# Kernel tuning notes

Hardware: AMD Instinct MI355X
Metric: run time of the kernel (lower is better)

The kernel has to match this reference:

```python
import jax, jax.numpy as jnp
import numpy as np

B, C, Himg, Wimg = 32, 256, 64, 64
P = 8            # partition (window) size
HEADS, DH = 8, 32
SEQ = P * P      # tokens per window = 64
SCALE = C ** (-0.5)  # note: feat_dim**-0.5, as in the source
EPS = 1e-5


def _relative_position_index(h, w):
    coords = np.stack(np.meshgrid(np.arange(h), np.arange(w), indexing='ij'))  # [2,h,w]
    cf = coords.reshape(2, -1)
    rel = cf[:, :, None] - cf[:, None, :]            # [2,hw,hw]
    rel = rel.transpose(1, 2, 0)
    rel[:, :, 0] += h - 1
    rel[:, :, 1] += w - 1
    rel[:, :, 0] *= 2 * w - 1
    return rel.sum(-1)                               # [hw,hw] int

REL_IDX = jnp.asarray(_relative_position_index(P, P).reshape(-1))  # [SEQ*SEQ]


def layernorm(x, g, b):
    mu = jnp.mean(x, -1, keepdims=True)
    var = jnp.mean(jnp.square(x - mu), -1, keepdims=True)
    return (x - mu) * jax.lax.rsqrt(var + EPS) * g + b


def setup_inputs() -> dict:
    key = jax.random.key(0)
    ks = jax.random.split(key, 12)
    d = {}
    d['x'] = jax.random.normal(ks[0], (B, C, Himg, Wimg), jnp.float32)
    d['ln1_g'] = jnp.ones((C,), jnp.float32)
    d['ln1_b'] = jnp.zeros((C,), jnp.float32)
    d['qkv_w'] = jax.random.normal(ks[1], (C, 3 * C), jnp.float32) * 0.02
    d['qkv_b'] = jnp.zeros((3 * C,), jnp.float32)
    d['merge_w'] = jax.random.normal(ks[2], (C, C), jnp.float32) * 0.02
    d['merge_b'] = jnp.zeros((C,), jnp.float32)
    d['bias_table'] = jax.random.normal(ks[3], ((2 * P - 1) * (2 * P - 1), HEADS), jnp.float32) * 0.02
    d['ln2_g'] = jnp.ones((C,), jnp.float32)
    d['ln2_b'] = jnp.zeros((C,), jnp.float32)
    d['mlp_w1'] = jax.random.normal(ks[4], (C, 4 * C), jnp.float32) * 0.02
    d['mlp_b1'] = jnp.zeros((4 * C,), jnp.float32)
    d['mlp_w2'] = jax.random.normal(ks[5], (4 * C, C), jnp.float32) * 0.02
    d['mlp_b2'] = jnp.zeros((C,), jnp.float32)
    return d


def reference(x, ln1_g, ln1_b, qkv_w, qkv_b, merge_w, merge_b, bias_table,
              ln2_g, ln2_b, mlp_w1, mlp_b1, mlp_w2, mlp_b2):
    Bn, Cn, H, W = x.shape
    hp, wp = H // P, W // P
    # window partition: [B,C,H,W] -> [B, G, P*P, C]
    xw = x.reshape(Bn, Cn, hp, P, wp, P).transpose(0, 2, 4, 3, 5, 1)
    xw = xw.reshape(Bn, hp * wp, P * P, Cn)

    # --- attention block ---
    h = layernorm(xw, ln1_g, ln1_b)
    qkv = h @ qkv_w + qkv_b                                    # [B,G,S,3C]
    q, k, v = jnp.split(qkv, 3, axis=-1)
    def heads(t):
        return t.reshape(Bn, hp * wp, SEQ, HEADS, DH).transpose(0, 1, 3, 2, 4)
    q, k, v = heads(q), heads(k) * SCALE, heads(v)             # [B,G,h,S,d]
    scores = jnp.einsum('bghid,bghjd->bghij', q, k)            # [B,G,h,S,S]
    rel_bias = bias_table[REL_IDX].reshape(SEQ, SEQ, HEADS).transpose(2, 0, 1)
    attn = jax.nn.softmax(scores + rel_bias[None, None], axis=-1)
    out = jnp.einsum('bghij,bghjd->bghid', attn, v)            # [B,G,h,S,d]
    out = out.transpose(0, 1, 3, 2, 4).reshape(Bn, hp * wp, SEQ, Cn)
    xw = xw + (out @ merge_w + merge_b)

    # --- MLP block ---
    h = layernorm(xw, ln2_g, ln2_b)
    h = jax.nn.gelu(h @ mlp_w1 + mlp_b1, approximate=False)
    xw = xw + (h @ mlp_w2 + mlp_b2)

    # window departition: [B,G,P*P,C] -> [B,C,H,W]
    y = xw.reshape(Bn, hp, wp, P, P, Cn).transpose(0, 5, 1, 3, 2, 4)
    return y.reshape(Bn, Cn, hp * P, wp * P)
```

## Files before the change

kernel.cpp:

```cpp
#include <hip/hip_runtime.h>

typedef __attribute__((ext_vector_type(8))) short short8;
typedef __attribute__((ext_vector_type(4))) short short4v;
typedef __attribute__((ext_vector_type(8))) unsigned short ushort8v;
typedef __attribute__((ext_vector_type(4))) float f32x4;
typedef __attribute__((ext_vector_type(4))) int int4v;
typedef __attribute__((ext_vector_type(4))) unsigned short ushort4v;
typedef __attribute__((ext_vector_type(2))) unsigned short ushort2v;

#define SCALE_F 0.0625f
#define EPS_F 1e-5f

__device__ __forceinline__ float bf2f(unsigned short u) {
  unsigned int i = ((unsigned int)u) << 16;
  return __builtin_bit_cast(float, i);
}
__device__ __forceinline__ unsigned short f2bf(float f) {
  unsigned int i = __builtin_bit_cast(unsigned int, f);
  i += 0x7fffu + ((i >> 16) & 1u);
  return (unsigned short)(i >> 16);
}

__device__ __forceinline__ float fast_gelu(float v) {
  float s = v * v;
  float u = v * __builtin_fmaf(s, 0.0713548163f, 1.5957691216f);
  float e = __expf(u);
  float r = __builtin_amdgcn_rcpf(e + 1.f);
  return v - v * r;
}

__device__ __forceinline__ void gload_lds16(const unsigned short* g, unsigned short* l) {
  __builtin_amdgcn_global_load_lds(
      (const __attribute__((address_space(1))) void*)g,
      (__attribute__((address_space(3))) void*)l, 16, 0, 0);
}

template<int K, int N>
__global__ void cast_wt(const float* __restrict__ src, unsigned short* __restrict__ dst) {
  int id = blockIdx.x * 256 + threadIdx.x;
  if (id >= K * N) return;
  int k = id % K, n = id / K;
  dst[id] = f2bf(src[(size_t)k * N + n]);
}

__global__ void build_relb(const float* __restrict__ table, float* __restrict__ relb) {
  int id = blockIdx.x * 256 + threadIdx.x;
  int h = id >> 12, i = (id >> 6) & 63, j = id & 63;
  int dy = (i >> 3) - (j >> 3) + 7;
  int dx = (i & 7) - (j & 7) + 7;
  relb[id] = table[(dy * 15 + dx) * 8 + h];
}

#define PLN_RS 264
__global__ __launch_bounds__(256) void part_ln1(
    const float* __restrict__ x, const float* __restrict__ g, const float* __restrict__ bb,
    unsigned short* __restrict__ h) {
  __shared__ __align__(16) unsigned short t_lds[128 * PLN_RS];
  __shared__ float ps_sum[128][2];
  __shared__ float ps_ss[128][2];
  const int tid = threadIdx.x;
  const int bid = blockIdx.x;
  const int b = bid >> 5, wr = (bid >> 2) & 7, cp = bid & 3;
  const int r0 = wr * 8;
  const int c0 = cp * 16;

  const int q = tid & 3, r = (tid >> 2) & 7, cb = tid >> 5;
  const float* xb = x + (size_t)b * 256 * 4096 + (size_t)(r0 + r) * 64 + c0 + q * 4;
#pragma unroll
  for (int it = 0; it < 16; it++) {
    int cpair = it * 8 + cb;
    const float* p0 = xb + (size_t)(2 * cpair) * 4096;
    f32x4 v0 = *(const f32x4*)p0;
    f32x4 v1 = *(const f32x4*)(p0 + 4096);
#pragma unroll
    for (int j = 0; j < 4; j++) {
      int px = r * 16 + q * 4 + j;
      ushort2v u = { f2bf(v0[j]), f2bf(v1[j]) };
      *(ushort2v*)(&t_lds[px * PLN_RS + 2 * cpair]) = u;
    }
  }
  __syncthreads();

  {
    const int p = tid & 127, half = tid >> 7;
    float sum = 0.f, ss = 0.f;
#pragma unroll
    for (int i = 0; i < 16; i++) {
      ushort8v u = *(const ushort8v*)(&t_lds[p * PLN_RS + half * 128 + i * 8]);
#pragma unroll
      for (int e = 0; e < 8; e++) { float f = bf2f(u[e]); sum += f; ss += f * f; }
    }
    ps_sum[p][half] = sum;
    ps_ss[p][half] = ss;
  }
  __syncthreads();

#pragma unroll
  for (int w = 0; w < 16; w++) {
    int id = w * 256 + tid;
    int p = id >> 5, ch = id & 31;
    float mu = (ps_sum[p][0] + ps_sum[p][1]) * (1.f / 256.f);
    float var = (ps_ss[p][0] + ps_ss[p][1]) * (1.f / 256.f) - mu * mu;
    float rs = rsqrtf(var + EPS_F);
    ushort8v u = *(const ushort8v*)(&t_lds[p * PLN_RS + ch * 8]);
    f32x4 g0 = *(const f32x4*)(g + ch * 8);
    f32x4 g1 = *(const f32x4*)(g + ch * 8 + 4);
    f32x4 b0 = *(const f32x4*)(bb + ch * 8);
    f32x4 b1 = *(const f32x4*)(bb + ch * 8 + 4);
    ushort8v o;
#pragma unroll
    for (int e = 0; e < 4; e++) {
      o[e]     = f2bf((bf2f(u[e])     - mu) * rs * g0[e] + b0[e]);
      o[e + 4] = f2bf((bf2f(u[e + 4]) - mu) * rs * g1[e] + b1[e]);
    }
    int rr = p >> 4, col = p & 15;
    size_t m = (size_t)b * 4096 + (size_t)(wr * 8 + cp * 2 + (col >> 3)) * 64 + rr * 8 + (col & 7);
    *(ushort8v*)(h + m * 256 + ch * 8) = o;
  }
}

__global__ __launch_bounds__(256) void ln2k(
    const unsigned short* __restrict__ x2, const float* __restrict__ g, const float* __restrict__ bb,
    unsigned short* __restrict__ h2) {
  int m = blockIdx.x * 4 + (threadIdx.x >> 6);
  int l = threadIdx.x & 63;
  ushort4v u = *(const ushort4v*)(x2 + (size_t)m * 256 + l * 4);
  float v[4];
  float sum = 0.f, ss = 0.f;
#pragma unroll
  for (int j = 0; j < 4; j++) { v[j] = bf2f(u[j]); sum += v[j]; ss += v[j] * v[j]; }
#pragma unroll
  for (int d = 1; d < 64; d <<= 1) {
    sum += __shfl_xor(sum, d, 64);
    ss  += __shfl_xor(ss, d, 64);
  }
  float mu = sum * (1.f / 256.f);
  float var = ss * (1.f / 256.f) - mu * mu;
  float rs = rsqrtf(var + EPS_F);
  ushort4v oh;
#pragma unroll
  for (int j = 0; j < 4; j++) {
    int c = l * 4 + j;
    oh[j] = f2bf((v[j] - mu) * rs * g[c] + bb[c]);
  }
  *(ushort4v*)(h2 + (size_t)m * 256 + l * 4) = oh;
}

enum { EPI_QKV = 0, EPI_MERGE = 1 };

template<int EPI>
__device__ __forceinline__ void gemm_body(
    unsigned short* As, unsigned short* Bs,
    const unsigned short* __restrict__ A, const unsigned short* __restrict__ Bt,
    const float* __restrict__ bias, const void* __restrict__ res,
    void* __restrict__ out, int K, int N, long m_base) {
  const int tid = threadIdx.x;
  const int l15 = tid & 15, lhi = (tid & 63) >> 4;
  const int wid = tid >> 6, wm = wid >> 1, wn = wid & 1;
  const size_t m0 = (size_t)blockIdx.x * 128;
  const int n0 = blockIdx.y * 128;
  const int row_s = tid >> 3, kc8 = (tid & 7) * 8;

  auto stage = [&](int kb, int k0) {
#pragma unroll
    for (int i = 0; i < 4; i++) {
      int row = i * 32 + row_s;
      gload_lds16(A + (m0 + row) * (size_t)K + k0 + kc8, &As[kb * 8192 + (i * 256 + tid) * 8]);
      gload_lds16(Bt + (size_t)(n0 + row) * (size_t)K + k0 + kc8, &Bs[kb * 8192 + (i * 256 + tid) * 8]);
    }
  };

  f32x4 acc[4][4];
#pragma unroll
  for (int i = 0; i < 4; i++)
#pragma unroll
    for (int j = 0; j < 4; j++) acc[i][j] = (f32x4){0.f, 0.f, 0.f, 0.f};

  stage(0, 0);
  int kb = 0;
  for (int k0 = 0; k0 < K; k0 += 64, kb ^= 1) {
    if (k0 + 64 < K) {
      stage(kb ^ 1, k0 + 64);
      asm volatile("s_waitcnt vmcnt(8)" ::: "memory");
    } else {
      asm volatile("s_waitcnt vmcnt(0)" ::: "memory");
    }
    __builtin_amdgcn_s_barrier();
#pragma unroll
    for (int ks = 0; ks < 2; ks++) {
      short8 af[4], bfr[4];
#pragma unroll
      for (int t = 0; t < 4; t++) {
        af[t]  = *(const short8*)(&As[kb * 8192 + (wm * 64 + t * 16 + l15) * 64 + ks * 32 + lhi * 8]);
        bfr[t] = *(const short8*)(&Bs[kb * 8192 + (wn * 64 + t * 16 + l15) * 64 + ks * 32 + lhi * 8]);
      }
#pragma unroll
      for (int mt = 0; mt < 4; mt++)
#pragma unroll
        for (int nt = 0; nt < 4; nt++)
          acc[mt][nt] = __builtin_amdgcn_mfma_f32_16x16x32_bf16(af[mt], bfr[nt], acc[mt][nt], 0, 0, 0);
    }
    __builtin_amdgcn_s_barrier();
  }

#pragma unroll
  for (int mt = 0; mt < 4; mt++) {
#pragma unroll
    for (int nt = 0; nt < 4; nt++) {
      const size_t gml0 = m0 + wm * 64 + mt * 16 + lhi * 4;
      const size_t gm0 = gml0 + (size_t)m_base;
      const int gn = n0 + wn * 64 + nt * 16 + l15;
      if (EPI == EPI_QKV) {
#pragma unroll
        for (int r = 0; r < 4; r++)
          ((unsigned short*)out)[(gml0 + r) * (size_t)N + gn] = f2bf(acc[mt][nt][r] + bias[gn]);
      } else {
        int bi = (int)(gm0 >> 12), gg = (int)((gm0 >> 6) & 63), s0 = (int)(gm0 & 63);
        size_t sp = (size_t)((gg >> 3) * 8 + (s0 >> 3)) * 64 + (gg & 7) * 8 + (s0 & 7);
        f32x4 xr = *(const f32x4*)(&((const float*)res)[((size_t)(bi * 256 + gn)) * 4096 + sp]);
#pragma unroll
        for (int r = 0; r < 4; r++)
          ((unsigned short*)out)[(gm0 + r) * 256 + gn] = f2bf(acc[mt][nt][r] + bias[gn] + xr[r]);
      }
    }
  }
}

#define GEMM_WRAP(name, epi)                                                          \
__global__ __launch_bounds__(256) void name(                                          \
    const unsigned short* __restrict__ A, const unsigned short* __restrict__ Bt,      \
    const float* __restrict__ bias, const void* __restrict__ res,                     \
    void* __restrict__ out, int K, int N, long m_base) {                              \
  __shared__ __align__(16) unsigned short As[2 * 128 * 64];                           \
  __shared__ __align__(16) unsigned short Bs[2 * 128 * 64];                           \
  gemm_body<epi>(As, Bs, A, Bt, bias, res, out, K, N, m_base);                        \
}
GEMM_WRAP(gemm_qkv, EPI_QKV)
GEMM_WRAP(gemm_merge, EPI_MERGE)

#define A2S 132
__global__ __launch_bounds__(256, 2) void mlp_fused(
    const unsigned short* __restrict__ h2, const unsigned short* __restrict__ w1t,
    const float* __restrict__ b1, const unsigned short* __restrict__ w2t,
    const float* __restrict__ b2, const unsigned short* __restrict__ x2,
    float* __restrict__ out) {
  __shared__ __align__(16) unsigned short Ash[64 * 256];
  __shared__ __align__(16) unsigned short A2sh[2][64 * A2S];
  const int tid = threadIdx.x;
  const int wid = tid >> 6, l = tid & 63, l15 = l & 15, lhi = l >> 4;
  const size_t m0 = (size_t)blockIdx.x * 64;

#pragma unroll
  for (int i = 0; i < 8; i++) {
    int uidx = i * 256 + tid;
    int row = uidx >> 5, su = uidx & 31;
    int gu = su ^ ((row & 15) << 1);
    gload_lds16(h2 + (m0 + row) * 256 + gu * 8, &Ash[uidx * 8]);
  }
  asm volatile("s_waitcnt vmcnt(0)" ::: "memory");
  __builtin_amdgcn_s_barrier();

  f32x4 oacc[4][4];
#pragma unroll
  for (int i = 0; i < 4; i++)
#pragma unroll
    for (int j = 0; j < 4; j++) oacc[i][j] = (f32x4){0.f, 0.f, 0.f, 0.f};

  auto gemm1_mfma = [&](short8 w1f[8][2], f32x4 hacc[4][2]) {
#pragma unroll
    for (int i = 0; i < 4; i++) {
      hacc[i][0] = (f32x4){0.f, 0.f, 0.f, 0.f};
      hacc[i][1] = (f32x4){0.f, 0.f, 0.f, 0.f};
    }
    __builtin_amdgcn_s_setprio(1);
#pragma unroll
    for (int kst = 0; kst < 8; kst++) {
      short8 af[4];
#pragma unroll
      for (int mt = 0; mt < 4; mt++) {
        int su = (kst * 4 + lhi) ^ ((l15 & 15) << 1);
        af[mt] = *(const short8*)(&Ash[(mt * 16 + l15) * 256 + su * 8]);
      }
#pragma unroll
      for (int mt = 0; mt < 4; mt++)
#pragma unroll
        for (int nt = 0; nt < 2; nt++)
          hacc[mt][nt] = __builtin_amdgcn_mfma_f32_16x16x32_bf16(af[mt], w1f[kst][nt], hacc[mt][nt], 0, 0, 0);
    }
    __builtin_amdgcn_s_setprio(0);
  };

  auto load_w1 = [&](int hs, short8 w1f[8][2]) {
    const int hc0 = hs * 128 + wid * 32;
#pragma unroll
    for (int kst = 0; kst < 8; kst++)
#pragma unroll
      for (int nt = 0; nt < 2; nt++)
        w1f[kst][nt] = *(const short8*)(w1t + (size_t)(hc0 + nt * 16 + l15) * 256 + kst * 32 + lhi * 8);
  };

  auto gelu_store = [&](int hs, int buf, f32x4 hacc[4][2]) {
    const int hc0 = hs * 128 + wid * 32;
    float bv0 = b1[hc0 + l15], bv1 = b1[hc0 + 16 + l15];
#pragma unroll
    for (int mt = 0; mt < 4; mt++)
#pragma unroll
      for (int nt = 0; nt < 2; nt++) {
        float bv = nt ? bv1 : bv0;
        int kh = wid * 32 + nt * 16 + l15;
#pragma unroll
        for (int rr = 0; rr < 4; rr++) {
          float v = hacc[mt][nt][rr] + bv;
          A2sh[buf][(mt * 16 + lhi * 4 + rr) * A2S + kh] = f2bf(fast_gelu(v));
        }
      }
  };

  auto gemm2 = [&](int hs, int buf) {
#pragma unroll
    for (int k2 = 0; k2 < 4; k2++) {
      short8 a2[4], bf2v[4];
#pragma unroll
      for (int mt = 0; mt < 4; mt++) {
        const unsigned short* p = &A2sh[buf][(mt * 16 + l15) * A2S + k2 * 32 + lhi * 8];
        short4v lo = *(const short4v*)p;
        short4v hi = *(const short4v*)(p + 4);
        a2[mt] = (short8){lo[0], lo[1], lo[2], lo[3], hi[0], hi[1], hi[2], hi[3]};
      }
#pragma unroll
      for (int nt = 0; nt < 4; nt++)
        bf2v[nt] = *(const short8*)(w2t + (size_t)(wid * 64 + nt * 16 + l15) * 1024 +
                                    hs * 128 + k2 * 32 + lhi * 8);
      __builtin_amdgcn_s_setprio(1);
#pragma unroll
      for (int mt = 0; mt < 4; mt++)
#pragma unroll
        for (int nt = 0; nt < 4; nt++)
          oacc[mt][nt] = __builtin_amdgcn_mfma_f32_16x16x32_bf16(a2[mt], bf2v[nt], oacc[mt][nt], 0, 0, 0);
      __builtin_amdgcn_s_setprio(0);
    }
  };

  {
    short8 w1f[8][2];
    f32x4 hacc[4][2];
    load_w1(0, w1f);
    gemm1_mfma(w1f, hacc);
    gelu_store(0, 0, hacc);
  }
  __builtin_amdgcn_s_barrier();

  for (int s = 0; s < 8; s++) {
    int buf = s & 1;
    if (s < 7) {
      short8 w1f[8][2];
      f32x4 hacc[4][2];
      load_w1(s + 1, w1f);
      gemm2(s, buf);
      gemm1_mfma(w1f, hacc);
      gelu_store(s + 1, buf ^ 1, hacc);
    } else {
      gemm2(s, buf);
    }
    __builtin_amdgcn_s_barrier();
  }

#pragma unroll
  for (int mt = 0; mt < 4; mt++) {
#pragma unroll
    for (int nt = 0; nt < 4; nt++) {
      size_t gm0 = m0 + mt * 16 + lhi * 4;
      int gn = wid * 64 + nt * 16 + l15;
      int bi = (int)(gm0 >> 12), gg = (int)((gm0 >> 6) & 63), s0 = (int)(gm0 & 63);
      size_t sp = (size_t)((gg >> 3) * 8 + (s0 >> 3)) * 64 + (gg & 7) * 8 + (s0 & 7);
      f32x4 o4;
#pragma unroll
      for (int r = 0; r < 4; r++)
        o4[r] = oacc[mt][nt][r] + b2[gn] + bf2f(x2[(gm0 + r) * 256 + gn]);
      *(f32x4*)(&out[((size_t)(bi * 256 + gn)) * 4096 + sp]) = o4;
    }
  }
}

__global__ __launch_bounds__(64) void attn_k(
    const unsigned short* __restrict__ qkv, const float* __restrict__ relb,
    unsigned short* __restrict__ o) {
  __shared__ __align__(16) unsigned short p_lds[64 * 72];
  __shared__ __align__(16) unsigned short vt_lds[32 * 72];
  const int l = threadIdx.x;
  const int l15 = l & 15, lhi = l >> 4;
  const int w = blockIdx.x, head = blockIdx.y;
  const unsigned short* base = qkv + (size_t)w * 64 * 768 + head * 32;

  short8 aq[4], bk[4];
#pragma unroll
  for (int t = 0; t < 4; t++) {
    aq[t] = *(const short8*)(base + (t * 16 + l15) * 768 + lhi * 8);
    bk[t] = *(const short8*)(base + 256 + (t * 16 + l15) * 768 + lhi * 8);
  }
  f32x4 s[4][4];
#pragma unroll
  for (int i = 0; i < 4; i++)
#pragma unroll
    for (int j = 0; j < 4; j++) s[i][j] = (f32x4){0.f, 0.f, 0.f, 0.f};
#pragma unroll
  for (int mt = 0; mt < 4; mt++)
#pragma unroll
    for (int nt = 0; nt < 4; nt++)
      s[mt][nt] = __builtin_amdgcn_mfma_f32_16x16x32_bf16(aq[mt], bk[nt], s[mt][nt], 0, 0, 0);

  const float* rb = relb + head * 4096;
  float rsum[4][4];
#pragma unroll
  for (int mt = 0; mt < 4; mt++) {
#pragma unroll
    for (int r = 0; r < 4; r++) {
      int row = mt * 16 + lhi * 4 + r;
      float vv[4];
      float vmax = -1e30f;
#pragma unroll
      for (int nt = 0; nt < 4; nt++) {
        int col = nt * 16 + l15;
        float v = s[mt][nt][r] * SCALE_F + rb[row * 64 + col];
        vv[nt] = v;
        vmax = fmaxf(vmax, v);
      }
#pragma unroll
      for (int d = 1; d < 16; d <<= 1) vmax = fmaxf(vmax, __shfl_xor(vmax, d, 64));
      float sum = 0.f;
#pragma unroll
      for (int nt = 0; nt < 4; nt++) {
        float p = __expf(vv[nt] - vmax);
        sum += p;
        p_lds[row * 72 + nt * 16 + l15] = f2bf(p);
      }
#pragma unroll
      for (int d = 1; d < 16; d <<= 1) sum += __shfl_xor(sum, d, 64);
      rsum[mt][r] = 1.f / sum;
    }
  }

#pragma unroll
  for (int j = 0; j < 4; j++) {
    short8 vv = *(const short8*)(base + 512 + l * 768 + j * 8);
#pragma unroll
    for (int e = 0; e < 8; e++)
      vt_lds[(j * 8 + e) * 72 + l] = (unsigned short)vv[e];
  }
  __syncthreads();

  f32x4 o2[4][2];
#pragma unroll
  for (int i = 0; i < 4; i++) { o2[i][0] = (f32x4){0.f,0.f,0.f,0.f}; o2[i][1] = (f32x4){0.f,0.f,0.f,0.f}; }
#pragma unroll
  for (int ks = 0; ks < 2; ks++) {
    short8 ap[4], bv[2];
#pragma unroll
    for (int t = 0; t < 4; t++)
      ap[t] = *(const short8*)(&p_lds[(t * 16 + l15) * 72 + ks * 32 + lhi * 8]);
#pragma unroll
    for (int t = 0; t < 2; t++)
      bv[t] = *(const short8*)(&vt_lds[(t * 16 + l15) * 72 + ks * 32 + lhi * 8]);
#pragma unroll
    for (int mt = 0; mt < 4; mt++)
#pragma unroll
      for (int n2 = 0; n2 < 2; n2++)
        o2[mt][n2] = __builtin_amdgcn_mfma_f32_16x16x32_bf16(ap[mt], bv[n2], o2[mt][n2], 0, 0, 0);
  }
#pragma unroll
  for (int mt = 0; mt < 4; mt++)
#pragma unroll
    for (int n2 = 0; n2 < 2; n2++)
#pragma unroll
      for (int r = 0; r < 4; r++) {
        int row = mt * 16 + lhi * 4 + r;
        int dh = n2 * 16 + l15;
        o[((size_t)w * 64 + row) * 256 + head * 32 + dh] = f2bf(o2[mt][n2][r] * rsum[mt][r]);
      }
}

extern "C" void kernel_launch(void* const* d_in, const int* in_sizes, int n_in,
                              void* d_out, int out_size, void* d_ws, size_t ws_size,
                              hipStream_t stream) {
  (void)in_sizes; (void)n_in; (void)out_size;
  const float* x          = (const float*)d_in[0];
  const float* ln1_g      = (const float*)d_in[1];
  const float* ln1_b      = (const float*)d_in[2];
  const float* qkv_w      = (const float*)d_in[3];
  const float* qkv_b      = (const float*)d_in[4];
  const float* merge_w    = (const float*)d_in[5];
  const float* merge_b    = (const float*)d_in[6];
  const float* bias_table = (const float*)d_in[7];
  const float* ln2_g      = (const float*)d_in[8];
  const float* ln2_b      = (const float*)d_in[9];
  const float* mlp_w1     = (const float*)d_in[10];
  const float* mlp_b1     = (const float*)d_in[11];
  const float* mlp_w2     = (const float*)d_in[12];
  const float* mlp_b2     = (const float*)d_in[13];

  const size_t MB = 1024ull * 1024ull;
  char* ws = (char*)d_ws;
  unsigned short* buf0 = (unsigned short*)(ws);
  unsigned short* x2   = (unsigned short*)(ws + 64 * MB);
  unsigned short* wqkv = (unsigned short*)(ws + 128 * MB);
  unsigned short* wmrg = wqkv + 768 * 256;
  unsigned short* w1t  = wmrg + 256 * 256;
  unsigned short* w2t  = w1t + 1024 * 256;
  float* relb          = (float*)(w2t + 256 * 1024);
  unsigned short* Cbuf = (unsigned short*)(ws + 130 * MB);

  size_t avail = ws_size > 130 * MB ? ws_size - 130 * MB : 0;
  int wc = 64;
  {
    const int cands[3] = {512, 256, 128};
    for (int i = 0; i < 3; i++)
      if ((size_t)cands[i] * 64 * 768 * 2 <= avail) { wc = cands[i]; break; }
  }

  cast_wt<256, 768><<<768, 256, 0, stream>>>(qkv_w, wqkv);
  cast_wt<256, 256><<<256, 256, 0, stream>>>(merge_w, wmrg);
  cast_wt<256, 1024><<<1024, 256, 0, stream>>>(mlp_w1, w1t);
  cast_wt<1024, 256><<<1024, 256, 0, stream>>>(mlp_w2, w2t);
  build_relb<<<128, 256, 0, stream>>>(bias_table, relb);

  part_ln1<<<1024, 256, 0, stream>>>(x, ln1_g, ln1_b, buf0);

  for (int w0 = 0; w0 < 2048; w0 += wc) {
    gemm_qkv<<<dim3(wc * 64 / 128, 6), 256, 0, stream>>>(
        buf0 + (size_t)w0 * 64 * 256, wqkv, qkv_b, nullptr, Cbuf, 256, 768, 0);
    attn_k<<<dim3(wc, 8), 64, 0, stream>>>(Cbuf, relb, buf0 + (size_t)w0 * 64 * 256);
  }

  gemm_merge<<<dim3(1024, 2), 256, 0, stream>>>(
      buf0, wmrg, merge_b, x, x2, 256, 256, 0);

  ln2k<<<32768, 256, 0, stream>>>(x2, ln2_g, ln2_b, buf0);

  mlp_fused<<<2048, 256, 0, stream>>>(buf0, w1t, mlp_b1, w2t, mlp_b2, x2, (float*)d_out);
}
```

Before: 799.4 us.

## Fuse LayerNorm2 into the MLP kernel and load W1 fragments inline

Removes the separate ln2k kernel. The fused MLP kernel now loads raw x2 rows into LDS, computes the per-row mean and variance in place, and writes normalized bf16 back into the swizzled LDS layout. This drops one launch and a full write-then-read of the normalized activation buffer through global memory. It also stops prefetching a whole W1 slice into registers ahead of gemm2: W1 fragments are now loaded per k-step inside gemm1, and the launch-bounds occupancy hint is removed. That cuts register pressure, but it may expose W1 load latency that was previously overlapped with gemm2.

```diff
diff --git a/kernel.cpp b/kernel.cpp
--- a/kernel.cpp
+++ b/kernel.cpp
@@ -119,33 +119,6 @@
   }
 }
 
-__global__ __launch_bounds__(256) void ln2k(
-    const unsigned short* __restrict__ x2, const float* __restrict__ g, const float* __restrict__ bb,
-    unsigned short* __restrict__ h2) {
-  int m = blockIdx.x * 4 + (threadIdx.x >> 6);
-  int l = threadIdx.x & 63;
-  ushort4v u = *(const ushort4v*)(x2 + (size_t)m * 256 + l * 4);
-  float v[4];
-  float sum = 0.f, ss = 0.f;
-#pragma unroll
-  for (int j = 0; j < 4; j++) { v[j] = bf2f(u[j]); sum += v[j]; ss += v[j] * v[j]; }
-#pragma unroll
-  for (int d = 1; d < 64; d <<= 1) {
-    sum += __shfl_xor(sum, d, 64);
-    ss  += __shfl_xor(ss, d, 64);
-  }
-  float mu = sum * (1.f / 256.f);
-  float var = ss * (1.f / 256.f) - mu * mu;
-  float rs = rsqrtf(var + EPS_F);
-  ushort4v oh;
-#pragma unroll
-  for (int j = 0; j < 4; j++) {
-    int c = l * 4 + j;
-    oh[j] = f2bf((v[j] - mu) * rs * g[c] + bb[c]);
-  }
-  *(ushort4v*)(h2 + (size_t)m * 256 + l * 4) = oh;
-}
-
 enum { EPI_QKV = 0, EPI_MERGE = 1 };
 
 template<int EPI>
@@ -239,11 +212,11 @@
 GEMM_WRAP(gemm_merge, EPI_MERGE)
 
 #define A2S 132
-__global__ __launch_bounds__(256, 2) void mlp_fused(
-    const unsigned short* __restrict__ h2, const unsigned short* __restrict__ w1t,
+__global__ __launch_bounds__(256) void mlp_fused(
+    const unsigned short* __restrict__ x2, const unsigned short* __restrict__ w1t,
     const float* __restrict__ b1, const unsigned short* __restrict__ w2t,
-    const float* __restrict__ b2, const unsigned short* __restrict__ x2,
-    float* __restrict__ out) {
+    const float* __restrict__ b2, const float* __restrict__ ln2g,
+    const float* __restrict__ ln2b, float* __restrict__ out) {
   __shared__ __align__(16) unsigned short Ash[64 * 256];
   __shared__ __align__(16) unsigned short A2sh[2][64 * A2S];
   const int tid = threadIdx.x;
@@ -253,50 +226,79 @@
 #pragma unroll
   for (int i = 0; i < 8; i++) {
     int uidx = i * 256 + tid;
-    int row = uidx >> 5, su = uidx & 31;
-    int gu = su ^ ((row & 15) << 1);
-    gload_lds16(h2 + (m0 + row) * 256 + gu * 8, &Ash[uidx * 8]);
+    gload_lds16(x2 + m0 * 256 + uidx * 8, &Ash[uidx * 8]);
   }
   asm volatile("s_waitcnt vmcnt(0)" ::: "memory");
   __builtin_amdgcn_s_barrier();
 
+  {
+    const int row = wid * 16 + (l >> 2);
+    const int p = l & 3;
+    unsigned short* rp = &Ash[row * 256];
+    short8 u[8];
+#pragma unroll
+    for (int e = 0; e < 8; e++)
+      u[e] = *(const short8*)(rp + (p * 8 + e) * 8);
+    float sum = 0.f, ss = 0.f;
+#pragma unroll
+    for (int e = 0; e < 8; e++)
+#pragma unroll
+      for (int j = 0; j < 8; j++) {
+        float f = bf2f((unsigned short)u[e][j]);
+        sum += f; ss += f * f;
+      }
+    sum += __shfl_xor(sum, 1, 64); ss += __shfl_xor(ss, 1, 64);
+    sum += __shfl_xor(sum, 2, 64); ss += __shfl_xor(ss, 2, 64);
+    float mu = sum * (1.f / 256.f);
+    float var = ss * (1.f / 256.f) - mu * mu;
+    float rs = rsqrtf(var + EPS_F);
+    const int key = (row & 15) << 1;
+#pragma unroll
+    for (int e = 0; e < 8; e++) {
+      int gu = p * 8 + e;
+      ushort8v o;
+#pragma unroll
+      for (int j = 0; j < 8; j++) {
+        int c = gu * 8 + j;
+        o[j] = f2bf((bf2f((unsigned short)u[e][j]) - mu) * rs * ln2g[c] + ln2b[c]);
+      }
+      *(ushort8v*)(rp + (gu ^ key) * 8) = o;
+    }
+  }
+  __builtin_amdgcn_s_barrier();
+
   f32x4 oacc[4][4];
 #pragma unroll
   for (int i = 0; i < 4; i++)
 #pragma unroll
     for (int j = 0; j < 4; j++) oacc[i][j] = (f32x4){0.f, 0.f, 0.f, 0.f};
 
-  auto gemm1_mfma = [&](short8 w1f[8][2], f32x4 hacc[4][2]) {
+  auto gemm1 = [&](int hs, f32x4 hacc[4][2]) {
 #pragma unroll
     for (int i = 0; i < 4; i++) {
       hacc[i][0] = (f32x4){0.f, 0.f, 0.f, 0.f};
       hacc[i][1] = (f32x4){0.f, 0.f, 0.f, 0.f};
     }
-    __builtin_amdgcn_s_setprio(1);
+    const int hc0 = hs * 128 + wid * 32;
 #pragma unroll
     for (int kst = 0; kst < 8; kst++) {
-      short8 af[4];
+      short8 af[4], bf1[2];
 #pragma unroll
       for (int mt = 0; mt < 4; mt++) {
-        int su = (kst * 4 + lhi) ^ ((l15 & 15) << 1);
+        int su = (kst * 4 + lhi) ^ (l15 << 1);
         af[mt] = *(const short8*)(&Ash[(mt * 16 + l15) * 256 + su * 8]);
       }
 #pragma unroll
+      for (int nt = 0; nt < 2; nt++)
+        bf1[nt] = *(const short8*)(w1t + (size_t)(hc0 + nt * 16 + l15) * 256 + kst * 32 + lhi * 8);
+      __builtin_amdgcn_s_setprio(1);
+#pragma unroll
       for (int mt = 0; mt < 4; mt++)
 #pragma unroll
         for (int nt = 0; nt < 2; nt++)
-          hacc[mt][nt] = __builtin_amdgcn_mfma_f32_16x16x32_bf16(af[mt], w1f[kst][nt], hacc[mt][nt], 0, 0, 0);
-    }
-    __builtin_amdgcn_s_setprio(0);
-  };
-
-  auto load_w1 = [&](int hs, short8 w1f[8][2]) {
-    const int hc0 = hs * 128 + wid * 32;
-#pragma unroll
-    for (int kst = 0; kst < 8; kst++)
-#pragma unroll
-      for (int nt = 0; nt < 2; nt++)
-        w1f[kst][nt] = *(const short8*)(w1t + (size_t)(hc0 + nt * 16 + l15) * 256 + kst * 32 + lhi * 8);
+          hacc[mt][nt] = __builtin_amdgcn_mfma_f32_16x16x32_bf16(af[mt], bf1[nt], hacc[mt][nt], 0, 0, 0);
+      __builtin_amdgcn_s_setprio(0);
+    }
   };
 
   auto gelu_store = [&](int hs, int buf, f32x4 hacc[4][2]) {
@@ -342,25 +344,18 @@
   };
 
   {
-    short8 w1f[8][2];
     f32x4 hacc[4][2];
-    load_w1(0, w1f);
-    gemm1_mfma(w1f, hacc);
+    gemm1(0, hacc);
     gelu_store(0, 0, hacc);
   }
   __builtin_amdgcn_s_barrier();
 
   for (int s = 0; s < 8; s++) {
-    int buf = s & 1;
+    gemm2(s, s & 1);
     if (s < 7) {
-      short8 w1f[8][2];
       f32x4 hacc[4][2];
-      load_w1(s + 1, w1f);
-      gemm2(s, buf);
-      gemm1_mfma(w1f, hacc);
-      gelu_store(s + 1, buf ^ 1, hacc);
-    } else {
-      gemm2(s, buf);
+      gemm1(s + 1, hacc);
+      gelu_store(s + 1, (s + 1) & 1, hacc);
     }
     __builtin_amdgcn_s_barrier();
   }
@@ -534,7 +529,5 @@
   gemm_merge<<<dim3(1024, 2), 256, 0, stream>>>(
       buf0, wmrg, merge_b, x, x2, 256, 256, 0);
 
-  ln2k<<<32768, 256, 0, stream>>>(x2, ln2_g, ln2_b, buf0);
-
-  mlp_fused<<<2048, 256, 0, stream>>>(buf0, w1t, mlp_b1, w2t, mlp_b2, x2, (float*)d_out);
-}
+  mlp_fused<<<2048, 256, 0, stream>>>(x2, w1t, mlp_b1, w2t, mlp_b2, ln2_g, ln2_b, (float*)d_out);
+}
```

New measurement: 840.0 us. 5.1% more time.
